# Kernel tuning notes

Hardware: AMD Instinct MI355X
Metric: run time of the kernel (lower is better)

The kernel has to match this reference:

```python
import math
import jax, jax.numpy as jnp
import numpy as np


def _proj(x, w, b):
    # 1x1x1 Conv3d == pointwise channel matmul: (B,C,T,H,W) x (O,C) -> (B,O,T,H,W)
    return jnp.einsum('bcthw,oc->bothw', x, w) + b[None, :, None, None, None]


def setup_inputs() -> dict:
    key = jax.random.key(0)
    ks = jax.random.split(key, 16)
    B, C, T, H, W = 2, 64, 16, 14, 14
    CI = C // 2
    s_in = 1.0 / math.sqrt(C)
    s_out = 1.0 / math.sqrt(CI)
    inp = {'x': jax.random.normal(ks[0], (B, C, T, H, W), jnp.float32)}
    # QKV projections for spatial (s) and temporal (t) branches: (CI, C) weights
    pnames = ['qs', 'ks', 'vs', 'qt', 'kt', 'vt']
    for i, n in enumerate(pnames):
        inp['W' + n] = jax.random.normal(ks[1 + i], (CI, C), jnp.float32) * s_in
        inp['b' + n] = jax.random.normal(ks[7 + i], (CI,), jnp.float32) * 0.01
    # output projection W: (C, CI)
    inp['Ww'] = jax.random.normal(ks[13], (C, CI), jnp.float32) * s_out
    inp['bw'] = jax.random.normal(ks[14], (C,), jnp.float32) * 0.01
    return inp


def reference(x, Wqs, bqs, Wks, bks, Wvs, bvs, Wqt, bqt, Wkt, bkt, Wvt, bvt, Ww, bw):
    B, C, T, H, W = x.shape
    CI = Wqs.shape[0]
    N = CI * H * W  # flat dim after original's raw .view (mixes channel & spatial/time)
    scale = 1.0 / math.sqrt(T)

    # ---- spatial branch: .view(B, T, -1) raw reshape of (B,CI,T,H,W) ----
    qs = _proj(x, Wqs, bqs).reshape(B, T, N).transpose(0, 2, 1)   # (B,N,T)
    ks_ = _proj(x, Wks, bks).reshape(B, T, N)                     # (B,T,N)
    vs = _proj(x, Wvs, bvs).reshape(B, T, N).transpose(0, 2, 1)   # (B,N,T)
    attn_s = jax.nn.softmax(jnp.einsum('bnt,btm->bnm', qs, ks_) * scale, axis=-1)  # (B,N,N)
    ys = jnp.einsum('bnm,bmt->bnt', attn_s, vs)                   # (B,N,T)
    ys = ys.transpose(0, 2, 1).reshape(B, CI, T, H, W)

    # ---- temporal branch: .view(B, CI*H*W, -1) raw reshape ----
    qt = _proj(x, Wqt, bqt).reshape(B, N, T).transpose(0, 2, 1)   # (B,T,N)
    kt = _proj(x, Wkt, bkt).reshape(B, N, T)                      # (B,N,T)
    vt = _proj(x, Wvt, bvt).reshape(B, N, T).transpose(0, 2, 1)   # (B,T,N)
    attn_t = jax.nn.softmax(jnp.einsum('btn,bns->bts', qt, kt) * scale, axis=-1)  # (B,T,T)
    yt = jnp.einsum('bts,bsn->btn', attn_t, vt)                   # (B,T,N)
    yt = yt.transpose(0, 2, 1).reshape(B, CI, T, H, W)

    y = ys + yt
    return _proj(y, Ww, bw) + x
```

## Files before the change

kernel.cpp:

```cpp
#include <hip/hip_runtime.h>
#include <math.h>

#define S3   3136
#define PB   100352
#define XB   200704
#define NN   6272
#define TGC  49

typedef __attribute__((ext_vector_type(8))) short bf16x8;
typedef __attribute__((ext_vector_type(16))) float f32x16;
typedef __attribute__((ext_vector_type(4))) uint u32x4;

__device__ inline ushort f2bf(float f) {
    uint u = __float_as_uint(f);
    return (ushort)((u + 0x7FFFu + ((u >> 16) & 1u)) >> 16);
}

__device__ inline uint cvtpk(float lo, float hi) {
    uint r;
    asm("v_cvt_pk_bf16_f32 %0, %1, %2" : "=v"(r) : "v"(lo), "v"(hi));
    return r;
}

__device__ inline void swap32(uint &a, uint &b) {
    asm("v_permlane32_swap_b32 %0, %1" : "+v"(a), "+v"(b));
}

__global__ __launch_bounds__(256) void proj_kernel(
    const float* __restrict__ x,
    const float* __restrict__ W0, const float* __restrict__ b0,
    const float* __restrict__ W1, const float* __restrict__ b1,
    const float* __restrict__ W2, const float* __restrict__ b2,
    const float* __restrict__ W3, const float* __restrict__ b3,
    const float* __restrict__ W4, const float* __restrict__ b4,
    const float* __restrict__ W5, const float* __restrict__ b5,
    ushort* __restrict__ Qb, ushort* __restrict__ Kb, ushort* __restrict__ Vb,
    float* __restrict__ Qt, float* __restrict__ Kt, float* __restrict__ Vt)
{
    const float* Wp; const float* bp;
    switch (blockIdx.y) {
        case 0:  Wp = W0; bp = b0; break;
        case 1:  Wp = W1; bp = b1; break;
        case 2:  Wp = W2; bp = b2; break;
        case 3:  Wp = W3; bp = b3; break;
        case 4:  Wp = W4; bp = b4; break;
        default: Wp = W5; bp = b5; break;
    }
    int z = blockIdx.z;

    int gid = blockIdx.x * 256 + threadIdx.x;
    if (gid >= 2 * S3) return;
    int b = (gid >= S3) ? 1 : 0;
    int s = gid - b * S3;

    float xr[64];
    #pragma unroll
    for (int c = 0; c < 64; ++c) xr[c] = x[(size_t)b * XB + (size_t)c * S3 + s];

    float a[4];
    #pragma unroll
    for (int oo = 0; oo < 4; ++oo) {
        int o = z * 4 + oo;
        float acc = bp[o];
        #pragma unroll
        for (int c = 0; c < 64; ++c) acc = fmaf(Wp[o * 64 + c], xr[c], acc);
        a[oo] = acc;
    }

    if (blockIdx.y < 2) {
        const float sc = (blockIdx.y == 0) ? 0.36067376022224085f : 1.0f;
        ushort* ob = (blockIdx.y == 0) ? Qb : Kb;
        #pragma unroll
        for (int h = 0; h < 2; ++h) {
            int n = h * S3 + s;
            uint u0 = f2bf(a[0 + h] * sc) | ((uint)f2bf(a[2 + h] * sc) << 16);
            *(uint*)(ob + ((size_t)(b * NN + n) * 16 + z * 2)) = u0;
        }
    } else if (blockIdx.y == 2) {
        #pragma unroll
        for (int oo = 0; oo < 4; ++oo) {
            int o = z * 4 + oo;
            Vb[(size_t)(b * 16 + (o >> 1)) * NN + (o & 1) * S3 + s] = f2bf(a[oo]);
        }
    } else {
        float* op = (blockIdx.y == 3) ? Qt : (blockIdx.y == 4) ? Kt : Vt;
        #pragma unroll
        for (int oo = 0; oo < 4; ++oo)
            op[(size_t)b * PB + (size_t)(z * 4 + oo) * S3 + s] = a[oo];
    }
}

__global__ __launch_bounds__(256) void gram_kernel(
    const float* __restrict__ Qt, const float* __restrict__ Kt,
    float* __restrict__ Gp)
{
    __shared__ float qs[128 * 16], ks[128 * 16];
    int b = blockIdx.y;
    int c = blockIdx.x;
    size_t base = (size_t)b * PB + (size_t)c * 2048;
    for (int i = threadIdx.x; i < 512; i += 256) {
        ((float4*)qs)[i] = ((const float4*)(Qt + base))[i];
        ((float4*)ks)[i] = ((const float4*)(Kt + base))[i];
    }
    __syncthreads();
    int t = threadIdx.x >> 4, s = threadIdx.x & 15;
    float acc = 0.0f;
    #pragma unroll 8
    for (int n = 0; n < 128; ++n)
        acc = fmaf(qs[n * 16 + t], ks[n * 16 + s], acc);
    Gp[(size_t)(b * TGC + c) * 256 + threadIdx.x] = acc;
}

__global__ __launch_bounds__(512) void attn_merge_kernel(
    const ushort* __restrict__ Qb, const ushort* __restrict__ Kb,
    const ushort* __restrict__ Vb, const float* __restrict__ Gp,
    const float* __restrict__ Vt, const float* __restrict__ x,
    const float* __restrict__ Ww, const float* __restrict__ bw,
    float* __restrict__ out)
{
    __shared__ float Yred[8][17][32];
    __shared__ float Gpart[2][256];
    __shared__ float Lsh[256];
    __shared__ float Ash[16][17];
    __shared__ float Ysh[32][17];

    int b   = blockIdx.y;
    int s0  = blockIdx.x * 16;
    int tid = threadIdx.x;

    {
        int j = tid & 255, g = tid >> 8;
        float a = 0.0f;
        for (int c = g; c < TGC; c += 2)
            a += Gp[(size_t)(b * TGC + c) * 256 + j];
        Gpart[g][j] = a;
    }
    __syncthreads();
    if (tid < 256) Lsh[tid] = (Gpart[0][tid] + Gpart[1][tid]) * 0.25f;
    __syncthreads();
    if (tid < 16) {
        int t = tid;
        const float* Lr = &Lsh[t * 16];
        float mx = -1e30f;
        #pragma unroll
        for (int s = 0; s < 16; ++s) mx = fmaxf(mx, Lr[s]);
        float e[16]; float sm = 0.0f;
        #pragma unroll
        for (int s = 0; s < 16; ++s) { e[s] = __expf(Lr[s] - mx); sm += e[s]; }
        float inv = 1.0f / sm;
        #pragma unroll
        for (int s = 0; s < 16; ++s) Ash[s][t] = e[s] * inv;
    }

    int wave = __builtin_amdgcn_readfirstlane(tid >> 6);
    int lane = tid & 63;
    int col  = lane & 31;
    int h    = lane >> 5;
    int nq   = (col >> 4) * S3 + s0 + (col & 15);

    bf16x8 qf = *(const bf16x8*)(Qb + ((size_t)(b * NN + nq) * 16 + h * 8));

    const bf16x8 vzero = {0, 0, 0, 0, 0, 0, 0, 0};
    const bf16x8 vones = {16256, 16256, 16256, 16256, 16256, 16256, 16256, 16256};
    f32x16 yacc;
    #pragma unroll
    for (int r = 0; r < 16; ++r) yacc[r] = 0.0f;
    f32x16 zero16 = yacc;

    for (int i = wave; i < 196; i += 8) {
        int mb = i * 32;
        bf16x8 kf = *(const bf16x8*)(Kb + ((size_t)(b * NN + mb + col) * 16 + h * 8));
        bf16x8 vf0 = vzero, vf1 = vzero;
        if (col < 16) {
            const ushort* vp = Vb + ((size_t)(b * 16 + col) * NN + mb + h * 8);
            vf0 = *(const bf16x8*)(vp);
            vf1 = *(const bf16x8*)(vp + 16);
        } else if (col == 16) { vf0 = vones; vf1 = vones; }

        f32x16 st = __builtin_amdgcn_mfma_f32_32x32x16_bf16(kf, qf, zero16, 0, 0, 0);
        float pv[16];
        #pragma unroll
        for (int r = 0; r < 16; ++r) pv[r] = __builtin_amdgcn_exp2f(st[r]);

        uint X0 = cvtpk(pv[0],  pv[1]),  X1 = cvtpk(pv[2],  pv[3]);
        uint Y0 = cvtpk(pv[4],  pv[5]),  Y1 = cvtpk(pv[6],  pv[7]);
        uint X2 = cvtpk(pv[8],  pv[9]),  X3 = cvtpk(pv[10], pv[11]);
        uint Y2 = cvtpk(pv[12], pv[13]), Y3 = cvtpk(pv[14], pv[15]);
        swap32(X0, Y0); swap32(X1, Y1);
        swap32(X2, Y2); swap32(X3, Y3);
        u32x4 pb0 = {X0, X1, Y0, Y1};
        u32x4 pb1 = {X2, X3, Y2, Y3};

        yacc = __builtin_amdgcn_mfma_f32_32x32x16_bf16(
                   vf0, __builtin_bit_cast(bf16x8, pb0), yacc, 0, 0, 0);
        yacc = __builtin_amdgcn_mfma_f32_32x32x16_bf16(
                   vf1, __builtin_bit_cast(bf16x8, pb1), yacc, 0, 0, 0);
    }

    #pragma unroll
    for (int r = 0; r < 8; ++r) {
        int t = (r & 3) + 8 * (r >> 2) + 4 * h;
        Yred[wave][t][col] = yacc[r];
    }
    if (h == 0) Yred[wave][16][col] = yacc[8];
    __syncthreads();

    {
        int t    = tid >> 5;
        int c2   = tid & 31;
        float ysum = 0.0f, lsum = 0.0f;
        #pragma unroll
        for (int w = 0; w < 8; ++w) {
            ysum += Yred[w][t][c2];
            lsum += Yred[w][16][c2];
        }
        float ys = ysum / lsum;

        int t2   = c2 & 15;
        int half = c2 >> 4;
        const float4* vp = (const float4*)(Vt + (size_t)b * PB + (size_t)t * NN
                                           + (size_t)half * S3 + s0);
        float4 v0 = vp[0], v1 = vp[1], v2 = vp[2], v3 = vp[3];
        float yt = Ash[0][t2] * v0.x;
        yt = fmaf(Ash[1][t2],  v0.y, yt); yt = fmaf(Ash[2][t2],  v0.z, yt);
        yt = fmaf(Ash[3][t2],  v0.w, yt); yt = fmaf(Ash[4][t2],  v1.x, yt);
        yt = fmaf(Ash[5][t2],  v1.y, yt); yt = fmaf(Ash[6][t2],  v1.z, yt);
        yt = fmaf(Ash[7][t2],  v1.w, yt); yt = fmaf(Ash[8][t2],  v2.x, yt);
        yt = fmaf(Ash[9][t2],  v2.y, yt); yt = fmaf(Ash[10][t2], v2.z, yt);
        yt = fmaf(Ash[11][t2], v2.w, yt); yt = fmaf(Ash[12][t2], v3.x, yt);
        yt = fmaf(Ash[13][t2], v3.y, yt); yt = fmaf(Ash[14][t2], v3.z, yt);
        yt = fmaf(Ash[15][t2], v3.w, yt);

        Ysh[2 * t + half][t2] = ys + yt;
    }
    __syncthreads();

    {
        int s  = tid & 15;
        int cg = tid >> 4;
        #pragma unroll
        for (int kk = 0; kk < 2; ++kk) {
            int c = cg + kk * 32;
            float acc = bw[c];
            const float4* wr = (const float4*)(Ww + c * 32);
            #pragma unroll
            for (int cb = 0; cb < 8; ++cb) {
                float4 w4 = wr[cb];
                acc = fmaf(w4.x, Ysh[cb * 4 + 0][s], acc);
                acc = fmaf(w4.y, Ysh[cb * 4 + 1][s], acc);
                acc = fmaf(w4.z, Ysh[cb * 4 + 2][s], acc);
                acc = fmaf(w4.w, Ysh[cb * 4 + 3][s], acc);
            }
            size_t o = (size_t)b * XB + (size_t)c * S3 + s0 + s;
            out[o] = x[o] + acc;
        }
    }
}

extern "C" void kernel_launch(void* const* d_in, const int* in_sizes, int n_in,
                              void* d_out, int out_size, void* d_ws, size_t ws_size,
                              hipStream_t stream)
{
    const float* x   = (const float*)d_in[0];
    const float* Wqs = (const float*)d_in[1];  const float* bqs = (const float*)d_in[2];
    const float* Wks = (const float*)d_in[3];  const float* bks = (const float*)d_in[4];
    const float* Wvs = (const float*)d_in[5];  const float* bvs = (const float*)d_in[6];
    const float* Wqt = (const float*)d_in[7];  const float* bqt = (const float*)d_in[8];
    const float* Wkt = (const float*)d_in[9];  const float* bkt = (const float*)d_in[10];
    const float* Wvt = (const float*)d_in[11]; const float* bvt = (const float*)d_in[12];
    const float* Ww  = (const float*)d_in[13]; const float* bw  = (const float*)d_in[14];

    float* ws = (float*)d_ws;
    ushort* Qb = (ushort*)(ws);
    ushort* Kb = (ushort*)(ws + 100352);
    ushort* Vb = (ushort*)(ws + 200704);
    float* Qt  = ws + 301056;
    float* Kt  = ws + 501760;
    float* Vt  = ws + 702464;
    float* Gp  = ws + 903168;

    proj_kernel<<<dim3(25, 6, 8), 256, 0, stream>>>(
        x, Wqs, bqs, Wks, bks, Wvs, bvs, Wqt, bqt, Wkt, bkt, Wvt, bvt,
        Qb, Kb, Vb, Qt, Kt, Vt);

    gram_kernel<<<dim3(TGC, 2), 256, 0, stream>>>(Qt, Kt, Gp);

    attn_merge_kernel<<<dim3(196, 2), 512, 0, stream>>>(
        Qb, Kb, Vb, Gp, Vt, x, Ww, bw, (float*)d_out);
}
```

Before: 125.0 us.

## Fuse temporal Gram computation into attention kernel with atomic grid barrier

Removes the separate gram kernel. Each attention block now computes a partial 16x16 temporal Gram from its own 512-element slice of Qt/Kt and atomically adds it into a global buffer, then signals a per-batch counter. After the spatial MFMA work, each block spins until all 196 blocks of its batch have contributed, then computes the temporal softmax. This saves a kernel launch and the partial-sum readback, but it depends on all 392 blocks being co-resident, adds atomic contention and a memset, and replaces the deterministic Gram reduction with a float atomic-order one.

```diff
diff --git a/kernel.cpp b/kernel.cpp
--- a/kernel.cpp
+++ b/kernel.cpp
@@ -90,66 +90,44 @@
     }
 }
 
-__global__ __launch_bounds__(256) void gram_kernel(
-    const float* __restrict__ Qt, const float* __restrict__ Kt,
-    float* __restrict__ Gp)
+__global__ __launch_bounds__(512, 4) void attn_merge_kernel(
+    const ushort* __restrict__ Qb, const ushort* __restrict__ Kb,
+    const ushort* __restrict__ Vb, const float* __restrict__ Qt,
+    const float* __restrict__ Kt, float* __restrict__ Gp,
+    uint* __restrict__ cnt, const float* __restrict__ Vt,
+    const float* __restrict__ x, const float* __restrict__ Ww,
+    const float* __restrict__ bw, float* __restrict__ out)
 {
-    __shared__ float qs[128 * 16], ks[128 * 16];
-    int b = blockIdx.y;
-    int c = blockIdx.x;
-    size_t base = (size_t)b * PB + (size_t)c * 2048;
-    for (int i = threadIdx.x; i < 512; i += 256) {
-        ((float4*)qs)[i] = ((const float4*)(Qt + base))[i];
-        ((float4*)ks)[i] = ((const float4*)(Kt + base))[i];
-    }
-    __syncthreads();
-    int t = threadIdx.x >> 4, s = threadIdx.x & 15;
-    float acc = 0.0f;
-    #pragma unroll 8
-    for (int n = 0; n < 128; ++n)
-        acc = fmaf(qs[n * 16 + t], ks[n * 16 + s], acc);
-    Gp[(size_t)(b * TGC + c) * 256 + threadIdx.x] = acc;
-}
-
-__global__ __launch_bounds__(512) void attn_merge_kernel(
-    const ushort* __restrict__ Qb, const ushort* __restrict__ Kb,
-    const ushort* __restrict__ Vb, const float* __restrict__ Gp,
-    const float* __restrict__ Vt, const float* __restrict__ x,
-    const float* __restrict__ Ww, const float* __restrict__ bw,
-    float* __restrict__ out)
-{
-    __shared__ float Yred[8][17][32];
-    __shared__ float Gpart[2][256];
-    __shared__ float Lsh[256];
+    __shared__ float shpool[4352];
     __shared__ float Ash[16][17];
     __shared__ float Ysh[32][17];
+#define YR(w, t, c) shpool[(((w) * 17) + (t)) * 32 + (c)]
 
     int b   = blockIdx.y;
     int s0  = blockIdx.x * 16;
     int tid = threadIdx.x;
 
     {
-        int j = tid & 255, g = tid >> 8;
-        float a = 0.0f;
-        for (int c = g; c < TGC; c += 2)
-            a += Gp[(size_t)(b * TGC + c) * 256 + j];
-        Gpart[g][j] = a;
-    }
-    __syncthreads();
-    if (tid < 256) Lsh[tid] = (Gpart[0][tid] + Gpart[1][tid]) * 0.25f;
-    __syncthreads();
-    if (tid < 16) {
-        int t = tid;
-        const float* Lr = &Lsh[t * 16];
-        float mx = -1e30f;
-        #pragma unroll
-        for (int s = 0; s < 16; ++s) mx = fmaxf(mx, Lr[s]);
-        float e[16]; float sm = 0.0f;
-        #pragma unroll
-        for (int s = 0; s < 16; ++s) { e[s] = __expf(Lr[s] - mx); sm += e[s]; }
-        float inv = 1.0f / sm;
-        #pragma unroll
-        for (int s = 0; s < 16; ++s) Ash[s][t] = e[s] * inv;
+        float* qs = shpool;
+        float* ks = shpool + 512;
+        size_t gbase = (size_t)b * PB + (size_t)blockIdx.x * 512;
+        if (tid < 128)
+            ((float4*)qs)[tid] = ((const float4*)(Qt + gbase))[tid];
+        else if (tid < 256)
+            ((float4*)ks)[tid - 128] = ((const float4*)(Kt + gbase))[tid - 128];
+        __syncthreads();
+        if (tid < 256) {
+            int t = tid >> 4, s = tid & 15;
+            float acc = 0.0f;
+            #pragma unroll 8
+            for (int n = 0; n < 32; ++n)
+                acc = fmaf(qs[n * 16 + t], ks[n * 16 + s], acc);
+            atomicAdd(&Gp[b * 256 + tid], acc);
+        }
+        __syncthreads();
+        if (tid == 0)
+            __hip_atomic_fetch_add(&cnt[b], 1u, __ATOMIC_RELEASE,
+                                   __HIP_MEMORY_SCOPE_AGENT);
     }
 
     int wave = __builtin_amdgcn_readfirstlane(tid >> 6);
@@ -200,9 +178,36 @@
     #pragma unroll
     for (int r = 0; r < 8; ++r) {
         int t = (r & 3) + 8 * (r >> 2) + 4 * h;
-        Yred[wave][t][col] = yacc[r];
-    }
-    if (h == 0) Yred[wave][16][col] = yacc[8];
+        YR(wave, t, col) = yacc[r];
+    }
+    if (h == 0) YR(wave, 16, col) = yacc[8];
+    __syncthreads();
+
+    if (tid == 0) {
+        long polls = 0;
+        while (__hip_atomic_load(&cnt[b], __ATOMIC_RELAXED,
+                                 __HIP_MEMORY_SCOPE_AGENT) < 196u) {
+            __builtin_amdgcn_s_sleep(2);
+            if (++polls > 10000000L) break;
+        }
+        (void)__hip_atomic_load(&cnt[b], __ATOMIC_ACQUIRE,
+                                __HIP_MEMORY_SCOPE_AGENT);
+    }
+    __syncthreads();
+
+    if (tid < 16) {
+        int t = tid;
+        const float* Lr = &Gp[b * 256 + t * 16];
+        float mx = -1e30f;
+        #pragma unroll
+        for (int s = 0; s < 16; ++s) mx = fmaxf(mx, Lr[s] * 0.25f);
+        float e[16]; float sm = 0.0f;
+        #pragma unroll
+        for (int s = 0; s < 16; ++s) { e[s] = __expf(Lr[s] * 0.25f - mx); sm += e[s]; }
+        float inv = 1.0f / sm;
+        #pragma unroll
+        for (int s = 0; s < 16; ++s) Ash[s][t] = e[s] * inv;
+    }
     __syncthreads();
 
     {
@@ -211,8 +216,8 @@
         float ysum = 0.0f, lsum = 0.0f;
         #pragma unroll
         for (int w = 0; w < 8; ++w) {
-            ysum += Yred[w][t][c2];
-            lsum += Yred[w][16][c2];
+            ysum += YR(w, t, c2);
+            lsum += YR(w, 16, c2);
         }
         float ys = ysum / lsum;
 
@@ -255,6 +260,7 @@
             out[o] = x[o] + acc;
         }
     }
+#undef YR
 }
 
 extern "C" void kernel_launch(void* const* d_in, const int* in_sizes, int n_in,
@@ -278,13 +284,14 @@
     float* Kt  = ws + 501760;
     float* Vt  = ws + 702464;
     float* Gp  = ws + 903168;
+    uint*  cnt = (uint*)(ws + 903680);
+
+    hipMemsetAsync(Gp, 0, 512 * sizeof(float) + 2 * sizeof(uint), stream);
 
     proj_kernel<<<dim3(25, 6, 8), 256, 0, stream>>>(
         x, Wqs, bqs, Wks, bks, Wvs, bvs, Wqt, bqt, Wkt, bkt, Wvt, bvt,
         Qb, Kb, Vb, Qt, Kt, Vt);
 
-    gram_kernel<<<dim3(TGC, 2), 256, 0, stream>>>(Qt, Kt, Gp);
-
     attn_merge_kernel<<<dim3(196, 2), 512, 0, stream>>>(
-        Qb, Kb, Vb, Gp, Vt, x, Ww, bw, (float*)d_out);
-}
+        Qb, Kb, Vb, Qt, Kt, Gp, cnt, Vt, x, Ww, bw, (float*)d_out);
+}
```

New measurement: 130.9 us. 4.8% more time.
